# Performance work log

Measured on AMD Instinct MI355X. Metric: run time of the kernel, lower is better.

## Reference

```python
import jax, jax.numpy as jnp
import numpy as np

N_EMBD = 768
T_LEN = 4096
BATCH = 4
ATTN_SPAN = 256
LN_EPS = 1e-5
SCALE = float(np.sqrt(N_EMBD * ATTN_SPAN))


def _mlp(x, w1, b1, w2, b2):
    # Linear -> exact GELU -> Linear (weights stored [in, out])
    h = jax.nn.gelu(x @ w1 + b1, approximate=False)
    return h @ w2 + b2


def setup_inputs() -> dict:
    key = jax.random.key(0)
    ks = jax.random.split(key, 16)
    s = 1.0 / np.sqrt(N_EMBD)
    def lin(k):
        kw, kb = jax.random.split(k)
        w = jax.random.uniform(kw, (N_EMBD, N_EMBD), jnp.float32, -s, s)
        b = jax.random.uniform(kb, (N_EMBD,), jnp.float32, -s, s)
        return w, b
    qw1, qb1 = lin(ks[0]); qw2, qb2 = lin(ks[1])
    kw1, kb1 = lin(ks[2]); kw2, kb2 = lin(ks[3])
    vw1, vb1 = lin(ks[4]); vw2, vb2 = lin(ks[5])
    x = jax.random.normal(ks[6], (BATCH, T_LEN, N_EMBD), jnp.float32)
    return {
        'x': x,
        'qw1': qw1, 'qb1': qb1, 'qw2': qw2, 'qb2': qb2,
        'kw1': kw1, 'kb1': kb1, 'kw2': kw2, 'kb2': kb2,
        'vw1': vw1, 'vb1': vb1, 'vw2': vw2, 'vb2': vb2,
        'ln_w': jnp.ones((N_EMBD,), jnp.float32),
        'ln_b': jnp.zeros((N_EMBD,), jnp.float32),
    }


def reference(x, qw1, qb1, qw2, qb2, kw1, kb1, kw2, kb2,
              vw1, vb1, vw2, vb2, ln_w, ln_b):
    T = x.shape[1]
    q = _mlp(x, qw1, qb1, qw2, qb2)
    k = _mlp(x, kw1, kb1, kw2, kb2)
    v = _mlp(x, vw1, vb1, vw2, vb2)
    # full T x T scores then banded causal mask (no softmax), as in source
    scores = jnp.einsum('bid,bjd->bij', q, k) / SCALE
    idx = jnp.arange(T)
    diff = idx[:, None] - idx[None, :]  # i - j
    mask = ((diff >= 0) & (diff < ATTN_SPAN)).astype(scores.dtype)
    scores = scores * mask
    y = jnp.einsum('bij,bjd->bid', scores, v)
    mu = jnp.mean(y, axis=-1, keepdims=True)
    var = jnp.var(y, axis=-1, keepdims=True)
    return (y - mu) * jax.lax.rsqrt(var + LN_EPS) * ln_w + ln_b
```

## Files before the change

kernel.cpp:

```cpp
#include <hip/hip_runtime.h>

typedef _Float16 f16;
typedef _Float16 half8 __attribute__((ext_vector_type(8)));
typedef float float4v __attribute__((ext_vector_type(4)));

#define NE 768
#define N3 2304
#define TT 4096
#define NB 4
#define MM (NB*TT)
#define SPAN 256
#define JW 320

#define GLDS(g, l) __builtin_amdgcn_global_load_lds( \
    (const __attribute__((address_space(1))) void*)(g), \
    (__attribute__((address_space(3))) void*)(l), 16, 0, 0)

__device__ __forceinline__ float gelu_exact(float v){
  return 0.5f * v * (1.0f + erff(v * 0.70710678118654752440f));
}

struct alignas(8) H4 { f16 a,b,c,d; };

__global__ __launch_bounds__(256) void cvt_f16_k(const float* __restrict__ in,
                                                 f16* __restrict__ out, int n){
  int i = (blockIdx.x*256 + threadIdx.x)*4;
  if (i >= n) return;
  float4 v = *(const float4*)(in + i);
  H4 o; o.a=(f16)v.x; o.b=(f16)v.y; o.c=(f16)v.z; o.d=(f16)v.w;
  *(H4*)(out + i) = o;
}

__global__ __launch_bounds__(256) void transpose_w6_k(
    const float* __restrict__ w0, const float* __restrict__ w1,
    const float* __restrict__ w2, const float* __restrict__ w3,
    const float* __restrict__ w4, const float* __restrict__ w5,
    f16* __restrict__ wt1, f16* __restrict__ wt2){
  __shared__ float tile[32][33];
  int z = blockIdx.z;
  const float* W = z==0?w0 : z==1?w1 : z==2?w2 : z==3?w3 : z==4?w4 : w5;
  f16* Wt = (z<3 ? wt1 + (size_t)z*NE*NE : wt2 + (size_t)(z-3)*NE*NE);
  int tx = threadIdx.x & 31, ty = threadIdx.x >> 5;
  int bx = blockIdx.x * 32, by = blockIdx.y * 32;
  #pragma unroll
  for (int r=0;r<32;r+=8) tile[ty+r][tx] = W[(size_t)(by+ty+r)*NE + bx + tx];
  __syncthreads();
  #pragma unroll
  for (int r=0;r<32;r+=8) Wt[(size_t)(bx+ty+r)*NE + by + tx] = (f16)tile[tx][ty+r];
}

__global__ void packb_k(const float* __restrict__ a0, const float* __restrict__ a1,
                        const float* __restrict__ a2, const float* __restrict__ c0,
                        const float* __restrict__ c1, const float* __restrict__ c2,
                        float* __restrict__ o1, float* __restrict__ o2){
  int i = blockIdx.x*256 + threadIdx.x;
  if (i < N3){
    const float* s = (i<NE) ? a0 : (i<2*NE ? a1 : a2);
    o1[i] = s[i % NE];
  } else if (i < 2*N3){
    int k = i - N3;
    const float* s = (k<NE) ? c0 : (k<2*NE ? c1 : c2);
    o2[k] = s[k % NE];
  }
}

__device__ __forceinline__ void gemm_core(
    const f16* __restrict__ A, int lda,
    const f16* __restrict__ Bt,
    int brow, int bcol, f16* As, f16* Bs, float4v (&acc)[4][4])
{
  const int tid  = threadIdx.x;
  const int lane = tid & 63, wave = tid >> 6;
  const int l15 = lane & 15, lk = lane >> 4;
  const int wr = (wave >> 1)*64, wc = (wave & 1)*64;
  const int srow0 = wave*32 + (lane >> 2);
  const int sslot = lane & 3;
  const int fsw = (lk ^ ((l15 >> 1) & 3)) * 8;

  for (int k0 = 0; k0 < NE; k0 += 32){
    #pragma unroll
    for (int t=0; t<2; ++t){
      int r  = srow0 + t*16;
      int sw = (sslot ^ ((r >> 1) & 3)) * 8;
      GLDS(A  + (size_t)(brow + r)*lda + k0 + sw, As + (wave*32 + t*16)*32);
      GLDS(Bt + (size_t)(bcol + r)*NE  + k0 + sw, Bs + (wave*32 + t*16)*32);
    }
    __syncthreads();
    half8 af[4], bf[4];
    #pragma unroll
    for (int i=0;i<4;++i) af[i] = *(const half8*)&As[(wr + i*16 + l15)*32 + fsw];
    #pragma unroll
    for (int j=0;j<4;++j) bf[j] = *(const half8*)&Bs[(wc + j*16 + l15)*32 + fsw];
    #pragma unroll
    for (int i=0;i<4;++i)
      #pragma unroll
      for (int j=0;j<4;++j)
        acc[i][j] = __builtin_amdgcn_mfma_f32_16x16x32_f16(af[i], bf[j], acc[i][j], 0, 0, 0);
    __syncthreads();
  }
}

__global__ __launch_bounds__(256) void gemm_l1_k(
    const f16* __restrict__ A, const f16* __restrict__ Bt,
    const float* __restrict__ bias, f16* __restrict__ Out)
{
  __shared__ f16 smem[16384];
  float4v acc[4][4]{};
  const int bid = blockIdx.x;
  const int L = (bid & 7)*288 + (bid >> 3);
  const int brow = (L/18)*128, bcol = (L%18)*128;
  gemm_core(A, NE, Bt, brow, bcol, smem, smem + 4096, acc);

  const int tid = threadIdx.x, lane = tid & 63, wave = tid >> 6;
  const int l15 = lane & 15, lk = lane >> 4;
  const int wr = (wave >> 1)*64, wc = (wave & 1)*64;
  #pragma unroll
  for (int j=0;j<4;++j){
    int col = wc + j*16 + l15;
    float bv = bias[bcol + col];
    #pragma unroll
    for (int i=0;i<4;++i){
      #pragma unroll
      for (int r=0;r<4;++r){
        int row = wr + i*16 + lk*4 + r;
        smem[row*128 + (col ^ ((row&7)<<3))] = (f16)gelu_exact(acc[i][j][r] + bv);
      }
    }
  }
  __syncthreads();
  #pragma unroll
  for (int it=0; it<8; ++it){
    int idx = tid + it*256;
    int row = idx >> 4, cc = (idx & 15)*8;
    half8 v = *(const half8*)&smem[row*128 + (cc ^ ((row&7)<<3))];
    *(half8*)(Out + (size_t)(brow + row)*N3 + bcol + cc) = v;
  }
}

__global__ __launch_bounds__(256) void gemm_l2_k(
    const f16* __restrict__ H, const f16* __restrict__ wt2_all,
    const float* __restrict__ b2_all,
    f16* __restrict__ qh, f16* __restrict__ kh, f16* __restrict__ vt)
{
  __shared__ f16 smem[16384];
  float4v acc[4][4]{};
  const int z = blockIdx.z;
  const int bid = blockIdx.x;
  const int L = (bid & 7)*96 + (bid >> 3);
  const int brow = (L/6)*128, bcol = (L%6)*128;
  gemm_core(H + z*NE, N3, wt2_all + (size_t)z*NE*NE, brow, bcol, smem, smem + 4096, acc);

  const float* bias = b2_all + z*NE;
  const int tid = threadIdx.x, lane = tid & 63, wave = tid >> 6;
  const int l15 = lane & 15, lk = lane >> 4;
  const int wr = (wave >> 1)*64, wc = (wave & 1)*64;

  if (z < 2){
    f16* Out = z ? kh : qh;
    #pragma unroll
    for (int j=0;j<4;++j){
      int col = wc + j*16 + l15;
      float bv = bias[bcol + col];
      #pragma unroll
      for (int i=0;i<4;++i){
        #pragma unroll
        for (int r=0;r<4;++r){
          int row = wr + i*16 + lk*4 + r;
          smem[row*128 + (col ^ ((row&7)<<3))] = (f16)(acc[i][j][r] + bv);
        }
      }
    }
    __syncthreads();
    #pragma unroll
    for (int it=0; it<8; ++it){
      int idx = tid + it*256;
      int row = idx >> 4, cc = (idx & 15)*8;
      half8 v = *(const half8*)&smem[row*128 + (cc ^ ((row&7)<<3))];
      *(half8*)(Out + (size_t)(brow + row)*NE + bcol + cc) = v;
    }
  } else {
    #pragma unroll
    for (int j=0;j<4;++j){
      int cl = wc + j*16 + l15;
      float bv = bias[bcol + cl];
      #pragma unroll
      for (int i=0;i<4;++i){
        int r0 = wr + i*16 + lk*4;
        H4 p; p.a = (f16)(acc[i][j][0] + bv); p.b = (f16)(acc[i][j][1] + bv);
              p.c = (f16)(acc[i][j][2] + bv); p.d = (f16)(acc[i][j][3] + bv);
        *(H4*)&smem[cl*128 + (r0 ^ ((cl&7)<<3))] = p;
      }
    }
    __syncthreads();
    int b = brow / TT, t0 = brow % TT;
    #pragma unroll
    for (int it=0; it<8; ++it){
      int idx = tid + it*256;
      int col = idx >> 4, rc = (idx & 15)*8;
      half8 v = *(const half8*)&smem[col*128 + (rc ^ ((col&7)<<3))];
      *(half8*)(vt + (size_t)b*NE*TT + (size_t)(bcol + col)*TT + t0 + rc) = v;
    }
  }
}

__global__ __launch_bounds__(256) void attn_qk_k(
    const f16* __restrict__ Q, const f16* __restrict__ K, f16* __restrict__ S)
{
  __shared__ f16 Ks[JW*40];
  const int tid = threadIdx.x, lane = tid & 63, wave = tid >> 6;
  const int l15 = lane & 15, lk = lane >> 4;
  const int qt = blockIdx.x, b = blockIdx.y;
  const int rowbase = b*TT + qt*64;
  const int jbase = qt*64 - SPAN;
  const int qrow = rowbase + wave*16;

  float4v acc[20]{};

  for (int k0 = 0; k0 < NE; k0 += 32){
    #pragma unroll
    for (int it=0; it<5; ++it){
      int idx = tid + it*256;
      int r = idx >> 2, c = (idx & 3)*8;
      int j = jbase + r;
      half8 v{};
      if (j >= 0) v = *(const half8*)(K + (size_t)(b*TT + j)*NE + k0 + c);
      *(half8*)&Ks[r*40 + c] = v;
    }
    __syncthreads();
    half8 aq = *(const half8*)(Q + (size_t)(qrow + l15)*NE + k0 + lk*8);
    #pragma unroll
    for (int f=0; f<20; ++f){
      half8 bk = *(const half8*)&Ks[(f*16 + l15)*40 + lk*8];
      acc[f] = __builtin_amdgcn_mfma_f32_16x16x32_f16(aq, bk, acc[f], 0, 0, 0);
    }
    __syncthreads();
  }
  const float inv = 1.0f / 443.40500673763256f;
  #pragma unroll
  for (int f=0; f<20; ++f){
    int c = f*16 + l15;
    int jg = jbase + c;
    #pragma unroll
    for (int r=0;r<4;++r){
      int iloc = wave*16 + lk*4 + r;
      int d = (qt*64 + iloc) - jg;
      float v = (d >= 0 && d < SPAN) ? acc[f][r]*inv : 0.0f;
      S[(size_t)(rowbase + iloc)*JW + c] = (f16)v;
    }
  }
}

__global__ __launch_bounds__(256) void attn_pv_k(
    const f16* __restrict__ S, const f16* __restrict__ Vt, float* __restrict__ Y)
{
  __shared__ f16 Vs[64*328];
  const int tid = threadIdx.x, lane = tid & 63, wave = tid >> 6;
  const int l15 = lane & 15, lk = lane >> 4;
  const int qt = blockIdx.x, dc = blockIdx.y, b = blockIdx.z;
  const int d0 = dc*64;
  const int jbase = qt*64 - SPAN;
  const int rowbase = b*TT + qt*64;

  #pragma unroll
  for (int it=0; it<10; ++it){
    int idx = tid + it*256;
    int dd = idx / 40;
    int c = (idx - dd*40)*8;
    int j = jbase + c;
    half8 v{};
    if (j >= 0) v = *(const half8*)(Vt + ((size_t)b*NE + d0 + dd)*TT + j);
    *(half8*)&Vs[dd*328 + c] = v;
  }
  __syncthreads();

  float4v acc[4]{};
  const f16* srow = S + (size_t)(rowbase + wave*16 + l15)*JW;
  #pragma unroll
  for (int kt = 0; kt < JW; kt += 32){
    half8 as = *(const half8*)(srow + kt + lk*8);
    #pragma unroll
    for (int nf=0; nf<4; ++nf){
      half8 bv = *(const half8*)&Vs[(nf*16 + l15)*328 + kt + lk*8];
      acc[nf] = __builtin_amdgcn_mfma_f32_16x16x32_f16(as, bv, acc[nf], 0, 0, 0);
    }
  }
  #pragma unroll
  for (int nf=0; nf<4; ++nf){
    #pragma unroll
    for (int r=0;r<4;++r){
      int row = rowbase + wave*16 + lk*4 + r;
      Y[(size_t)row*NE + d0 + nf*16 + l15] = acc[nf][r];
    }
  }
}

__global__ __launch_bounds__(256) void layernorm_k(
    const float* __restrict__ Y, const float* __restrict__ g,
    const float* __restrict__ be, float* __restrict__ Out)
{
  int row  = blockIdx.x*4 + (threadIdx.x >> 6);
  int lane = threadIdx.x & 63;
  const float* y = Y + (size_t)row*NE;
  float v[12], s=0.f, s2=0.f;
  #pragma unroll
  for (int i=0;i<12;++i){ v[i] = y[lane + i*64]; s += v[i]; s2 += v[i]*v[i]; }
  #pragma unroll
  for (int m=32;m>=1;m>>=1){ s += __shfl_xor(s,m,64); s2 += __shfl_xor(s2,m,64); }
  float mu  = s*(1.f/NE);
  float var = s2*(1.f/NE) - mu*mu;
  float rs  = rsqrtf(var + 1e-5f);
  float* o = Out + (size_t)row*NE;
  #pragma unroll
  for (int i=0;i<12;++i){ int c = lane + i*64; o[c] = (v[i]-mu)*rs*g[c] + be[c]; }
}

extern "C" void kernel_launch(void* const* d_in, const int* in_sizes, int n_in,
                              void* d_out, int out_size, void* d_ws, size_t ws_size,
                              hipStream_t stream)
{
  (void)in_sizes; (void)n_in; (void)out_size; (void)ws_size;
  const float* x     = (const float*)d_in[0];
  const float* w1[3] = {(const float*)d_in[1], (const float*)d_in[5], (const float*)d_in[9]};
  const float* b1[3] = {(const float*)d_in[2], (const float*)d_in[6], (const float*)d_in[10]};
  const float* w2[3] = {(const float*)d_in[3], (const float*)d_in[7], (const float*)d_in[11]};
  const float* b2[3] = {(const float*)d_in[4], (const float*)d_in[8], (const float*)d_in[12]};
  const float* lnw = (const float*)d_in[13];
  const float* lnb = (const float*)d_in[14];

  char* ws = (char*)d_ws;
  size_t off = 0;
  auto alloc = [&](size_t bytes)->void* {
    void* p = ws + off; off += (bytes + 255) & ~size_t(255); return p;
  };
  f16* xh  = (f16*)alloc((size_t)MM*NE*2);
  f16* Ha  = (f16*)alloc((size_t)MM*N3*2);
  f16* qh  = (f16*)alloc((size_t)MM*NE*2);
  f16* kh  = (f16*)alloc((size_t)MM*NE*2);
  f16* vt  = (f16*)alloc((size_t)MM*NE*2);
  f16* wt1 = (f16*)alloc((size_t)N3*NE*2);
  f16* wt2 = (f16*)alloc((size_t)N3*NE*2);
  float* b1a = (float*)alloc((size_t)N3*4);
  float* b2a = (float*)alloc((size_t)N3*4);
  f16*   sb  = xh;
  float* y   = (float*)Ha;

  cvt_f16_k<<<(MM*NE/4 + 255)/256, 256, 0, stream>>>(x, xh, MM*NE);
  transpose_w6_k<<<dim3(NE/32, NE/32, 6), 256, 0, stream>>>(
      w1[0], w1[1], w1[2], w2[0], w2[1], w2[2], wt1, wt2);
  packb_k<<<18, 256, 0, stream>>>(b1[0], b1[1], b1[2], b2[0], b2[1], b2[2], b1a, b2a);

  gemm_l1_k<<<dim3(MM/128 * N3/128), 256, 0, stream>>>(xh, wt1, b1a, Ha);
  gemm_l2_k<<<dim3(MM/128 * NE/128, 1, 3), 256, 0, stream>>>(Ha, wt2, b2a, qh, kh, vt);

  attn_qk_k<<<dim3(TT/64, NB), 256, 0, stream>>>(qh, kh, sb);
  attn_pv_k<<<dim3(TT/64, NE/64, NB), 256, 0, stream>>>(sb, vt, y);
  layernorm_k<<<MM/4, 256, 0, stream>>>(y, lnw, lnb, (float*)d_out);
}
```

Before: 427.4 us.

## Double-buffer GEMM core with BK=64 and overlapped async LDS loads

Rewrites the shared GEMM main loop used by both MLP layers. K-tiles grow from 32 to 64 and are double-buffered in LDS, with the next tile's global-to-LDS loads issued before computing the current one. Explicit vmcnt waits and barriers replace the two __syncthreads per iteration, and a new XOR swizzle handles 64-wide rows. LDS per block doubles to 64 KB, which may reduce occupancy.

```diff
diff --git a/kernel.cpp b/kernel.cpp
--- a/kernel.cpp
+++ b/kernel.cpp
@@ -15,6 +15,10 @@
 #define GLDS(g, l) __builtin_amdgcn_global_load_lds( \
     (const __attribute__((address_space(1))) void*)(g), \
     (__attribute__((address_space(3))) void*)(l), 16, 0, 0)
+
+#define VMW(n) asm volatile("s_waitcnt vmcnt(" #n ")" ::: "memory")
+#define SBAR() __builtin_amdgcn_s_barrier()
+#define SCHED0() __builtin_amdgcn_sched_barrier(0)
 
 __device__ __forceinline__ float gelu_exact(float v){
   return 0.5f * v * (1.0f + erff(v * 0.70710678118654752440f));
@@ -66,50 +70,76 @@
 
 __device__ __forceinline__ void gemm_core(
     const f16* __restrict__ A, int lda,
-    const f16* __restrict__ Bt,
-    int brow, int bcol, f16* As, f16* Bs, float4v (&acc)[4][4])
-{
-  const int tid  = threadIdx.x;
-  const int lane = tid & 63, wave = tid >> 6;
+    const f16* __restrict__ Bt, int ldb,
+    int brow, int bcol, f16* sh, float4v (&acc)[4][4])
+{
+  const int tid = threadIdx.x, lane = tid & 63, wave = tid >> 6;
   const int l15 = lane & 15, lk = lane >> 4;
   const int wr = (wave >> 1)*64, wc = (wave & 1)*64;
-  const int srow0 = wave*32 + (lane >> 2);
-  const int sslot = lane & 3;
-  const int fsw = (lk ^ ((l15 >> 1) & 3)) * 8;
-
-  for (int k0 = 0; k0 < NE; k0 += 32){
-    #pragma unroll
-    for (int t=0; t<2; ++t){
-      int r  = srow0 + t*16;
-      int sw = (sslot ^ ((r >> 1) & 3)) * 8;
-      GLDS(A  + (size_t)(brow + r)*lda + k0 + sw, As + (wave*32 + t*16)*32);
-      GLDS(Bt + (size_t)(bcol + r)*NE  + k0 + sw, Bs + (wave*32 + t*16)*32);
-    }
-    __syncthreads();
-    half8 af[4], bf[4];
-    #pragma unroll
-    for (int i=0;i<4;++i) af[i] = *(const half8*)&As[(wr + i*16 + l15)*32 + fsw];
-    #pragma unroll
-    for (int j=0;j<4;++j) bf[j] = *(const half8*)&Bs[(wc + j*16 + l15)*32 + fsw];
+
+  const int srow   = wave*8 + (lane >> 3);
+  const int schunk = ((lane & 7) ^ (lane >> 3))*8;
+  const f16* Asrc = A  + (size_t)(brow + srow)*lda + schunk;
+  const f16* Bsrc = Bt + (size_t)(bcol + srow)*ldb + schunk;
+  const int wdst = wave*512;
+
+  const int rsw0 = (lk ^ (l15 & 7))*8;
+  const int rsw1 = ((4 + lk) ^ (l15 & 7))*8;
+
+#define STAGE(buf, k0) do{ \
+    f16* _a = sh + (buf)*16384 + wdst; \
+    f16* _b = _a + 8192; \
+    const f16* _as = Asrc + (k0); \
+    const f16* _bs = Bsrc + (k0); \
+    _Pragma("unroll") \
+    for (int _t = 0; _t < 4; ++_t){ \
+      GLDS(_as + (size_t)(_t*32)*lda, _a + _t*2048); \
+      GLDS(_bs + (size_t)(_t*32)*ldb, _b + _t*2048); \
+    } }while(0)
+
+  STAGE(0, 0);
+  #pragma unroll
+  for (int t = 0; t < 12; ++t){
+    const f16* Ac = sh + (t & 1)*16384;
+    const f16* Bc = Ac + 8192;
+    if (t < 11) STAGE((t+1) & 1, (t+1)*64);
+    if (t < 11) { VMW(8); } else { VMW(0); }
+    SBAR(); SCHED0();
+    half8 af0[4], af1[4], bf0[4], bf1[4];
+    #pragma unroll
+    for (int i=0;i<4;++i){
+      const f16* pa = Ac + (wr + i*16 + l15)*64;
+      af0[i] = *(const half8*)(pa + rsw0);
+      af1[i] = *(const half8*)(pa + rsw1);
+      const f16* pb = Bc + (wc + i*16 + l15)*64;
+      bf0[i] = *(const half8*)(pb + rsw0);
+      bf1[i] = *(const half8*)(pb + rsw1);
+    }
     #pragma unroll
     for (int i=0;i<4;++i)
       #pragma unroll
       for (int j=0;j<4;++j)
-        acc[i][j] = __builtin_amdgcn_mfma_f32_16x16x32_f16(af[i], bf[j], acc[i][j], 0, 0, 0);
-    __syncthreads();
-  }
+        acc[i][j] = __builtin_amdgcn_mfma_f32_16x16x32_f16(af0[i], bf0[j], acc[i][j], 0, 0, 0);
+    #pragma unroll
+    for (int i=0;i<4;++i)
+      #pragma unroll
+      for (int j=0;j<4;++j)
+        acc[i][j] = __builtin_amdgcn_mfma_f32_16x16x32_f16(af1[i], bf1[j], acc[i][j], 0, 0, 0);
+    SCHED0(); SBAR();
+  }
+#undef STAGE
 }
 
 __global__ __launch_bounds__(256) void gemm_l1_k(
     const f16* __restrict__ A, const f16* __restrict__ Bt,
     const float* __restrict__ bias, f16* __restrict__ Out)
 {
-  __shared__ f16 smem[16384];
+  __shared__ f16 smem[32768];
   float4v acc[4][4]{};
   const int bid = blockIdx.x;
   const int L = (bid & 7)*288 + (bid >> 3);
   const int brow = (L/18)*128, bcol = (L%18)*128;
-  gemm_core(A, NE, Bt, brow, bcol, smem, smem + 4096, acc);
+  gemm_core(A, NE, Bt, NE, brow, bcol, smem, acc);
 
   const int tid = threadIdx.x, lane = tid & 63, wave = tid >> 6;
   const int l15 = lane & 15, lk = lane >> 4;
@@ -142,13 +172,13 @@
     const float* __restrict__ b2_all,
     f16* __restrict__ qh, f16* __restrict__ kh, f16* __restrict__ vt)
 {
-  __shared__ f16 smem[16384];
+  __shared__ f16 smem[32768];
   float4v acc[4][4]{};
   const int z = blockIdx.z;
   const int bid = blockIdx.x;
   const int L = (bid & 7)*96 + (bid >> 3);
   const int brow = (L/6)*128, bcol = (L%6)*128;
-  gemm_core(H + z*NE, N3, wt2_all + (size_t)z*NE*NE, brow, bcol, smem, smem + 4096, acc);
+  gemm_core(H + z*NE, N3, wt2_all + (size_t)z*NE*NE, NE, brow, bcol, smem, acc);
 
   const float* bias = b2_all + z*NE;
   const int tid = threadIdx.x, lane = tid & 63, wave = tid >> 6;
```

Measured after the change: 408.3 us. 1.05x faster.
